# Kernel tuning notes

Measured on AMD Instinct MI355X. Metric: run time of the kernel, lower is better.

Reference implementation:

```python
import jax, jax.numpy as jnp
import numpy as np

B, N, DIM = 4, 2048, 512
HEADS, DK = 8, 64
SCALE = DK ** -0.5


def setup_inputs() -> dict:
    key = jax.random.key(0)
    k1, k2, k3, k4 = jax.random.split(key, 4)
    x = jax.random.normal(k1, (B, N, DIM), dtype=jnp.float32)
    # nn.Linear(dim, dim_key*heads, bias=False): y = x @ W.T; store W already transposed
    Wq = jax.random.normal(k2, (DIM, HEADS * DK), dtype=jnp.float32) * (DIM ** -0.5)
    Wk = jax.random.normal(k3, (DIM, HEADS * DK), dtype=jnp.float32) * (DIM ** -0.5)
    rel_content_bias = jax.random.normal(k4, (1, HEADS, 1, DK), dtype=jnp.float32)
    return {"x": x, "Wq": Wq, "Wk": Wk, "rel_content_bias": rel_content_bias}


def _split_heads(t, h):
    # [b, n, h*d] -> [b, h, n, d]
    b, n, hd = t.shape
    return t.reshape(b, n, h, hd // h).transpose(0, 2, 1, 3)


def reference(x, Wq, Wk, rel_content_bias):
    q = _split_heads(x @ Wq, HEADS) * SCALE          # [b, h, n, dk]
    k = _split_heads(x @ Wk, HEADS)                  # [b, h, n, dk]
    v = _split_heads(x, HEADS)                       # [b, h, n, dim/h]
    logits = jnp.einsum('bhid,bhjd->bhij', q + rel_content_bias, k)
    attn = jax.nn.sigmoid(logits)                    # no softmax normalization
    out = jnp.einsum('bhij,bhjd->bhid', attn, v)     # [b, h, n, dim/h]
    b, h, n, d = out.shape
    return out.transpose(0, 2, 1, 3).reshape(b, n, h * d)
```

## Files before the change

### kernel.cpp

```cpp
#include <hip/hip_runtime.h>
#include <hip/hip_bf16.h>
#include <stdint.h>

#define BB 4
#define NN 2048
#define DIMD 512
#define HH 8
#define DKK 64
#define MTOT (BB * NN)
constexpr float SCALE = 0.125f;
constexpr float L2E = 1.44269504089f;

typedef __attribute__((ext_vector_type(4))) float f32x4;
typedef __attribute__((ext_vector_type(2))) float f32x2;
typedef __attribute__((ext_vector_type(8))) short bf16x8;
typedef __attribute__((ext_vector_type(4))) _Float16 f16x4;
typedef __attribute__((ext_vector_type(8))) _Float16 f16x8;
typedef __attribute__((ext_vector_type(2))) __fp16 fp16v2;
typedef __attribute__((ext_vector_type(4))) __fp16 fp16v4;
typedef __attribute__((ext_vector_type(2))) unsigned int u32x2;

union pack8 { unsigned short s[8]; uint4 v; };
union fragu { u32x2 h[2]; bf16x8 v; };
union cat8u { f16x4 h[2]; f16x8 v; };

__device__ __forceinline__ unsigned short f2bf(float f) {
  union { float f; uint32_t u; } v; v.f = f;
  uint32_t u = v.u;
  return (unsigned short)((u + 0x7FFFu + ((u >> 16) & 1u)) >> 16);
}

__device__ __forceinline__ unsigned short f2h(float f) {
  union { _Float16 h; unsigned short u; } c; c.h = (_Float16)f;
  return c.u;
}

__device__ __forceinline__ bf16x8 ld_frag(const unsigned short* p) {
  fragu f;
  f.h[0] = *(const u32x2*)p;
  f.h[1] = *(const u32x2*)(p + 4);
  return f.v;
}
__device__ __forceinline__ void st8(unsigned short* p, uint4 v) {
  *(u32x2*)p = (u32x2){v.x, v.y};
  *(u32x2*)(p + 4) = (u32x2){v.z, v.w};
}

__device__ __forceinline__ f16x8 cat8(f16x4 a, f16x4 b) {
  cat8u u; u.h[0] = a; u.h[1] = b; return u.v;
}

__device__ __forceinline__ int kperm(int j) {
  return (j & 96) | ((j & 4) << 2) | ((j & 24) >> 1) | (j & 3);
}

__device__ __forceinline__ f16x4 sig_pack(f32x4 sv) {
  float e0 = __builtin_amdgcn_exp2f(-__builtin_fabsf(sv[0]));
  float e1 = __builtin_amdgcn_exp2f(-__builtin_fabsf(sv[1]));
  float e2 = __builtin_amdgcn_exp2f(-__builtin_fabsf(sv[2]));
  float e3 = __builtin_amdgcn_exp2f(-__builtin_fabsf(sv[3]));
  const f32x2 c3 = {-0.22184f, -0.22184f};
  const f32x2 c2 = {0.66550f, 0.66550f};
  const f32x2 c1 = {-0.94280f, -0.94280f};
  const f32x2 c0 = {0.49826f, 0.49826f};
  f32x2 eA = {e0, e1}, eB = {e2, e3};
  f32x2 pA = __builtin_elementwise_fma(
      __builtin_elementwise_fma(__builtin_elementwise_fma(c3, eA, c2), eA, c1),
      eA, c0);
  f32x2 pB = __builtin_elementwise_fma(
      __builtin_elementwise_fma(__builtin_elementwise_fma(c3, eB, c2), eB, c1),
      eB, c0);
  float r0 = __builtin_copysignf(pA.x, sv[0]);
  float r1 = __builtin_copysignf(pA.y, sv[1]);
  float r2 = __builtin_copysignf(pB.x, sv[2]);
  float r3 = __builtin_copysignf(pB.y, sv[3]);
  fp16v2 lo = __builtin_amdgcn_cvt_pkrtz(r0, r1);
  fp16v2 hi = __builtin_amdgcn_cvt_pkrtz(r2, r3);
  fp16v4 p;
  p.x = lo.x; p.y = lo.y; p.z = hi.x; p.w = hi.y;
  return __builtin_bit_cast(f16x4, p);
}

__global__ __launch_bounds__(256) void prep(const float* __restrict__ x,
                                            const float* __restrict__ wq,
                                            const float* __restrict__ wk,
                                            unsigned short* __restrict__ xtf,
                                            unsigned short* __restrict__ wtq,
                                            unsigned short* __restrict__ wtk,
                                            float* __restrict__ vsum_p) {
  const int bx = blockIdx.x, tid = threadIdx.x;
  if (bx < 256) {
    __shared__ float Pred[4][64];
    int q = bx;
    int b = q >> 6, r = q & 63;
    int dt = r >> 3, nt = r & 7;
    int dl = tid & 63, c = tid >> 6;
    int d = dt * 64 + dl;
    int n0 = nt * 256 + c * 64;
    const float* xp = x + ((size_t)b * NN + n0) * DIMD + d;
    unsigned short* dp = xtf + ((size_t)b * DIMD + d) * NN + n0;
    float s = 0.f;
#pragma unroll
    for (int g = 0; g < 8; g++) {
      pack8 pa;
#pragma unroll
      for (int k = 0; k < 8; k++) {
        float v = xp[(size_t)(g * 8 + k) * DIMD];
        s += v;
        pa.s[k] = f2h(v);
      }
      *(uint4*)(dp + g * 8) = pa.v;
    }
    Pred[c][dl] = s;
    __syncthreads();
    if (c == 0) {
      float t = Pred[0][dl] + Pred[1][dl] + Pred[2][dl] + Pred[3][dl];
      vsum_p[((size_t)b * 8 + nt) * DIMD + d] = t;
    }
  } else {
    __shared__ __align__(16) unsigned short T[64][68];
    int q = bx - 256;
    const float* w = (q >= 64) ? wk : wq;
    unsigned short* wt = (q >= 64) ? wtk : wtq;
    int r = q & 63;
    int kt = r >> 3, nt = r & 7;
    const int k0 = kt * 64, n0 = nt * 64;
#pragma unroll
    for (int rr = 0; rr < 16; rr++) {
      int idx = tid + rr * 256;
      int kl = idx >> 6, nl = idx & 63;
      T[nl][kl] = f2bf(w[(size_t)(k0 + kl) * DIMD + n0 + nl]);
    }
    __syncthreads();
#pragma unroll
    for (int rr = 0; rr < 2; rr++) {
      int idx = tid + rr * 256;
      int nl = idx >> 3, c = idx & 7;
      fragu f;
      f.h[0] = *(const u32x2*)&T[nl][c * 8];
      f.h[1] = *(const u32x2*)&T[nl][c * 8 + 4];
      uint4 v;
      v.x = f.h[0].x; v.y = f.h[0].y; v.z = f.h[1].x; v.w = f.h[1].y;
      *(uint4*)(wt + (size_t)(n0 + nl) * DIMD + k0 + c * 8) = v;
    }
  }
}

__global__ __launch_bounds__(512, 4) void qk_gemm(const float* __restrict__ x,
                                                  const unsigned short* __restrict__ wtq,
                                                  const unsigned short* __restrict__ wtk,
                                                  const float* __restrict__ bias,
                                                  unsigned short* __restrict__ qout,
                                                  unsigned short* __restrict__ kout) {
  __shared__ __align__(16) unsigned short Als[128][68];
  __shared__ __align__(16) unsigned short Bls[128][68];
  const int mb = blockIdx.x, nb = blockIdx.y;
  const bool isQ = (nb < 4);
  const unsigned short* wt = isQ ? wtq : wtk;
  unsigned short* outp = isQ ? qout : kout;
  const int n0 = (nb & 3) * 128, m0 = mb * 128;
  const int tid = threadIdx.x;
  const int wave = tid >> 6, lane = tid & 63;
  const int quad = lane >> 4, l16 = lane & 15;
  const int wm = wave >> 2, wn = wave & 3;

  f32x4 acc[4][2];
#pragma unroll
  for (int a = 0; a < 4; a++)
#pragma unroll
    for (int c = 0; c < 2; c++) acc[a][c] = (f32x4){0.f, 0.f, 0.f, 0.f};

  const int srow[2] = {tid >> 3, (tid + 512) >> 3};
  const int scol = (tid & 7) * 8;
  uint4 pa[2], pb[2];

  auto loadA = [&](int r, int k0) -> uint4 {
    const float* ap = x + (size_t)(m0 + srow[r]) * DIMD + k0 + scol;
    float4 a = *(const float4*)ap;
    float4 b = *(const float4*)(ap + 4);
    pack8 p;
    p.s[0] = f2bf(a.x); p.s[1] = f2bf(a.y); p.s[2] = f2bf(a.z); p.s[3] = f2bf(a.w);
    p.s[4] = f2bf(b.x); p.s[5] = f2bf(b.y); p.s[6] = f2bf(b.z); p.s[7] = f2bf(b.w);
    return p.v;
  };

#pragma unroll
  for (int r = 0; r < 2; r++) {
    pa[r] = loadA(r, 0);
    pb[r] = *(const uint4*)(wt + (size_t)(n0 + srow[r]) * DIMD + scol);
  }

  for (int k0 = 0; k0 < DIMD; k0 += 64) {
    __syncthreads();
#pragma unroll
    for (int r = 0; r < 2; r++) {
      st8(&Als[srow[r]][scol], pa[r]);
      st8(&Bls[srow[r]][scol], pb[r]);
    }
    __syncthreads();
    if (k0 + 64 < DIMD) {
#pragma unroll
      for (int r = 0; r < 2; r++) {
        pa[r] = loadA(r, k0 + 64);
        pb[r] = *(const uint4*)(wt + (size_t)(n0 + srow[r]) * DIMD + k0 + 64 + scol);
      }
    }
#pragma unroll
    for (int ks = 0; ks < 2; ks++) {
      bf16x8 af[4], bfr[2];
#pragma unroll
      for (int t = 0; t < 4; t++)
        af[t] = ld_frag(&Als[wm * 64 + t * 16 + l16][quad * 8 + ks * 32]);
#pragma unroll
      for (int t = 0; t < 2; t++)
        bfr[t] = ld_frag(&Bls[wn * 32 + t * 16 + l16][quad * 8 + ks * 32]);
#pragma unroll
      for (int tm = 0; tm < 4; tm++)
#pragma unroll
        for (int tn = 0; tn < 2; tn++)
          acc[tm][tn] =
              __builtin_amdgcn_mfma_f32_16x16x32_bf16(af[tm], bfr[tn], acc[tm][tn], 0, 0, 0);
    }
  }
#pragma unroll
  for (int tm = 0; tm < 4; tm++) {
#pragma unroll
    for (int tn = 0; tn < 2; tn++) {
      int gcol = n0 + wn * 32 + tn * 16 + l16;
      float bl = isQ ? bias[gcol] * L2E : 0.f;
#pragma unroll
      for (int r = 0; r < 4; r++) {
        int row = m0 + wm * 64 + tm * 16 + quad * 4 + r;
        float v = acc[tm][tn][r];
        if (isQ) v = v * (SCALE * L2E) + bl;
        outp[(size_t)row * DIMD + gcol] = f2bf(v);
      }
    }
  }
}

__global__ __launch_bounds__(512, 4) void attn(const unsigned short* __restrict__ qb,
                                               const unsigned short* __restrict__ kb,
                                               const unsigned short* __restrict__ xtf,
                                               const float* __restrict__ vsum_p,
                                               float* __restrict__ out) {
  __shared__ __align__(16) char smem[68608];
  unsigned short* Kall = (unsigned short*)smem;
  unsigned short* Vall = Kall + 2 * 128 * 68;
  float* R0 = (float*)smem;

  const int bh = blockIdx.x, it = blockIdx.y;
  const int b = bh >> 3, h = bh & 7;
  const int i0 = it * 128;
  const int tid = threadIdx.x;
  const int lane = tid & 63;
  const int grp = tid >> 8;
  const int wv = (tid >> 6) & 3;
  const int gtid = tid & 255;
  const int quad = lane >> 4, l16 = lane & 15;

  bf16x8 qf[2][2];
  int irow[2];
#pragma unroll
  for (int s_ = 0; s_ < 2; s_++) {
    irow[s_] = i0 + wv * 32 + s_ * 16 + l16;
    const unsigned short* qp = qb + ((size_t)b * NN + irow[s_]) * DIMD + h * DKK + quad * 8;
    qf[s_][0] = *(const bf16x8*)qp;
    qf[s_][1] = *(const bf16x8*)(qp + 32);
  }

  f32x4 o[2][4];
#pragma unroll
  for (int s_ = 0; s_ < 2; s_++)
#pragma unroll
    for (int td = 0; td < 4; td++) o[s_][td] = (f32x4){0.f, 0.f, 0.f, 0.f};

  const unsigned short* kbase = kb + (size_t)b * NN * DIMD + h * DKK;
  const unsigned short* vbase = xtf + ((size_t)b * DIMD + h * DKK) * NN;
  unsigned short* Kg = Kall + grp * (128 * 68);
  unsigned short* Vg = Vall + grp * (64 * 132);
  const int jbase = grp * 1024;

  const int krow = gtid >> 3, kcol = (gtid & 7) * 8;
  const int vrow = gtid >> 4, vcol = (gtid & 15) * 8;
  uint4 pk[4], pv[4];

  auto prefetch = [&](int t) {
    const int jb = jbase + t * 128;
#pragma unroll
    for (int r = 0; r < 4; r++) {
      pk[r] = *(const uint4*)(kbase + (size_t)(jb + krow + 32 * r) * DIMD + kcol);
      pv[r] = *(const uint4*)(vbase + (size_t)(vrow + 16 * r) * NN + jb + vcol);
    }
  };
  prefetch(0);

  for (int itr = 0; itr < 8; itr++) {
    __syncthreads();
#pragma unroll
    for (int r = 0; r < 4; r++) {
      st8(&Kg[kperm(krow + 32 * r) * 68 + kcol], pk[r]);
      st8(&Vg[(vrow + 16 * r) * 132 + vcol], pv[r]);
    }
    __syncthreads();
    if (itr < 7) prefetch(itr + 1);

    __builtin_amdgcn_s_setprio(1);
#pragma unroll
    for (int a = 0; a < 4; a++) {
      bf16x8 ke0 = ld_frag(&Kg[((2 * a) * 16 + l16) * 68 + quad * 8]);
      bf16x8 ke1 = ld_frag(&Kg[((2 * a) * 16 + l16) * 68 + quad * 8 + 32]);
      bf16x8 ko0 = ld_frag(&Kg[((2 * a + 1) * 16 + l16) * 68 + quad * 8]);
      bf16x8 ko1 = ld_frag(&Kg[((2 * a + 1) * 16 + l16) * 68 + quad * 8 + 32]);
      f16x8 pf[2];
#pragma unroll
      for (int s_ = 0; s_ < 2; s_++) {
        f32x4 se = (f32x4){0.f, 0.f, 0.f, 0.f};
        f32x4 so = (f32x4){0.f, 0.f, 0.f, 0.f};
        se = __builtin_amdgcn_mfma_f32_16x16x32_bf16(ke0, qf[s_][0], se, 0, 0, 0);
        se = __builtin_amdgcn_mfma_f32_16x16x32_bf16(ke1, qf[s_][1], se, 0, 0, 0);
        so = __builtin_amdgcn_mfma_f32_16x16x32_bf16(ko0, qf[s_][0], so, 0, 0, 0);
        so = __builtin_amdgcn_mfma_f32_16x16x32_bf16(ko1, qf[s_][1], so, 0, 0, 0);
        pf[s_] = cat8(sig_pack(se), sig_pack(so));
      }
#pragma unroll
      for (int td = 0; td < 4; td++) {
        f16x8 vf = __builtin_bit_cast(
            f16x8, ld_frag(&Vg[(td * 16 + l16) * 132 + a * 32 + quad * 8]));
        o[0][td] = __builtin_amdgcn_mfma_f32_16x16x32_f16(vf, pf[0], o[0][td], 0, 0, 0);
        o[1][td] = __builtin_amdgcn_mfma_f32_16x16x32_f16(vf, pf[1], o[1][td], 0, 0, 0);
      }
    }
    __builtin_amdgcn_s_setprio(0);
  }

  __syncthreads();
  if (grp == 1) {
#pragma unroll
    for (int s_ = 0; s_ < 2; s_++)
#pragma unroll
      for (int td = 0; td < 4; td++) {
        int base = (wv * 32 + s_ * 16 + l16) * 66 + td * 16 + quad * 4;
        *(f32x2*)&R0[base] = (f32x2){o[s_][td][0], o[s_][td][1]};
        *(f32x2*)&R0[base + 2] = (f32x2){o[s_][td][2], o[s_][td][3]};
      }
  }
  __syncthreads();
  if (grp == 0) {
    const float* vp = vsum_p + (size_t)b * 8 * DIMD + h * DKK;
    f32x4 vs[4];
#pragma unroll
    for (int td = 0; td < 4; td++) {
      f32x4 a = (f32x4){0.f, 0.f, 0.f, 0.f};
#pragma unroll
      for (int p = 0; p < 8; p++) {
        f32x4 t = *(const f32x4*)&vp[(size_t)p * DIMD + td * 16 + quad * 4];
        a[0] += t[0]; a[1] += t[1]; a[2] += t[2]; a[3] += t[3];
      }
      vs[td] = a;
    }
#pragma unroll
    for (int s_ = 0; s_ < 2; s_++) {
#pragma unroll
      for (int td = 0; td < 4; td++) {
        int base = (wv * 32 + s_ * 16 + l16) * 66 + td * 16 + quad * 4;
        f32x2 a = *(const f32x2*)&R0[base];
        f32x2 c = *(const f32x2*)&R0[base + 2];
        o[s_][td][0] += a.x + 0.5f * vs[td][0];
        o[s_][td][1] += a.y + 0.5f * vs[td][1];
        o[s_][td][2] += c.x + 0.5f * vs[td][2];
        o[s_][td][3] += c.y + 0.5f * vs[td][3];
        float* op = out + ((size_t)b * NN + irow[s_]) * DIMD + h * DKK + td * 16 + quad * 4;
        *(f32x4*)op = o[s_][td];
      }
    }
  }
}

extern "C" void kernel_launch(void* const* d_in, const int* in_sizes, int n_in,
                              void* d_out, int out_size, void* d_ws, size_t ws_size,
                              hipStream_t stream) {
  const float* x = (const float*)d_in[0];
  const float* Wq = (const float*)d_in[1];
  const float* Wk = (const float*)d_in[2];
  const float* bias = (const float*)d_in[3];
  float* out = (float*)d_out;

  unsigned short* ws = (unsigned short*)d_ws;
  unsigned short* xtf = ws;
  unsigned short* wtq = xtf + (size_t)MTOT * DIMD;
  unsigned short* wtk = wtq + (size_t)DIMD * DIMD;
  unsigned short* qb = wtk + (size_t)DIMD * DIMD;
  unsigned short* kb = qb + (size_t)MTOT * DIMD;
  float* vsum_p = (float*)(kb + (size_t)MTOT * DIMD);

  prep<<<dim3(384), 256, 0, stream>>>(x, Wq, Wk, xtf, wtq, wtk, vsum_p);
  qk_gemm<<<dim3(64, 8), 512, 0, stream>>>(x, wtq, wtk, bias, qb, kb);
  attn<<<dim3(32, 16), 512, 0, stream>>>(qb, kb, xtf, vsum_p, out);
}
```

Measured before the change: 154.2 us.

## Move x transpose/vsum into GEMM launch and double-buffer K fragment loads

The x transpose to fp16 and the column-sum work move out of the prep kernel into extra blocks of the qk_gemm grid, so prep only converts the weights and that work overlaps with the GEMM. In the attention inner loop, K fragments are loaded one step ahead into alternating register sets so LDS reads overlap the MFMA work. The extra grid rows share the GEMM's launch bounds and LDS allocation, which may change occupancy, and the ping-pong buffers raise register pressure.

```diff
diff --git a/kernel.cpp b/kernel.cpp
--- a/kernel.cpp
+++ b/kernel.cpp
@@ -81,85 +81,87 @@
   return __builtin_bit_cast(f16x4, p);
 }
 
-__global__ __launch_bounds__(256) void prep(const float* __restrict__ x,
-                                            const float* __restrict__ wq,
-                                            const float* __restrict__ wk,
-                                            unsigned short* __restrict__ xtf,
-                                            unsigned short* __restrict__ wtq,
-                                            unsigned short* __restrict__ wtk,
-                                            float* __restrict__ vsum_p) {
-  const int bx = blockIdx.x, tid = threadIdx.x;
-  if (bx < 256) {
-    __shared__ float Pred[4][64];
-    int q = bx;
+__global__ __launch_bounds__(256) void prep_w(const float* __restrict__ wq,
+                                              const float* __restrict__ wk,
+                                              unsigned short* __restrict__ wtq,
+                                              unsigned short* __restrict__ wtk) {
+  __shared__ __align__(16) unsigned short T[64][68];
+  const int tid = threadIdx.x;
+  int q = blockIdx.x;
+  const float* w = (q >= 64) ? wk : wq;
+  unsigned short* wt = (q >= 64) ? wtk : wtq;
+  int r = q & 63;
+  int kt = r >> 3, nt = r & 7;
+  const int k0 = kt * 64, n0 = nt * 64;
+#pragma unroll
+  for (int rr = 0; rr < 16; rr++) {
+    int idx = tid + rr * 256;
+    int kl = idx >> 6, nl = idx & 63;
+    T[nl][kl] = f2bf(w[(size_t)(k0 + kl) * DIMD + n0 + nl]);
+  }
+  __syncthreads();
+#pragma unroll
+  for (int rr = 0; rr < 2; rr++) {
+    int idx = tid + rr * 256;
+    int nl = idx >> 3, c = idx & 7;
+    fragu f;
+    f.h[0] = *(const u32x2*)&T[nl][c * 8];
+    f.h[1] = *(const u32x2*)&T[nl][c * 8 + 4];
+    uint4 v;
+    v.x = f.h[0].x; v.y = f.h[0].y; v.z = f.h[1].x; v.w = f.h[1].y;
+    *(uint4*)(wt + (size_t)(n0 + nl) * DIMD + k0 + c * 8) = v;
+  }
+}
+
+__global__ __launch_bounds__(512, 4) void qk_gemm(const float* __restrict__ x,
+                                                  const unsigned short* __restrict__ wtq,
+                                                  const unsigned short* __restrict__ wtk,
+                                                  const float* __restrict__ bias,
+                                                  unsigned short* __restrict__ qout,
+                                                  unsigned short* __restrict__ kout,
+                                                  unsigned short* __restrict__ xtf,
+                                                  float* __restrict__ vsum_p) {
+  const int mb = blockIdx.x, nb = blockIdx.y;
+  const int tid = threadIdx.x;
+
+  if (nb >= 8) {
+    __shared__ float Pred[2][4][64];
+    const int g = tid >> 8, t = tid & 255;
+    int q = (mb * 2 + (nb - 8)) * 2 + g;
     int b = q >> 6, r = q & 63;
     int dt = r >> 3, nt = r & 7;
-    int dl = tid & 63, c = tid >> 6;
+    int dl = t & 63, c = t >> 6;
     int d = dt * 64 + dl;
     int n0 = nt * 256 + c * 64;
     const float* xp = x + ((size_t)b * NN + n0) * DIMD + d;
     unsigned short* dp = xtf + ((size_t)b * DIMD + d) * NN + n0;
     float s = 0.f;
 #pragma unroll
-    for (int g = 0; g < 8; g++) {
+    for (int gg = 0; gg < 8; gg++) {
       pack8 pa;
 #pragma unroll
       for (int k = 0; k < 8; k++) {
-        float v = xp[(size_t)(g * 8 + k) * DIMD];
+        float v = xp[(size_t)(gg * 8 + k) * DIMD];
         s += v;
         pa.s[k] = f2h(v);
       }
-      *(uint4*)(dp + g * 8) = pa.v;
-    }
-    Pred[c][dl] = s;
+      *(uint4*)(dp + gg * 8) = pa.v;
+    }
+    Pred[g][c][dl] = s;
     __syncthreads();
     if (c == 0) {
-      float t = Pred[0][dl] + Pred[1][dl] + Pred[2][dl] + Pred[3][dl];
-      vsum_p[((size_t)b * 8 + nt) * DIMD + d] = t;
-    }
-  } else {
-    __shared__ __align__(16) unsigned short T[64][68];
-    int q = bx - 256;
-    const float* w = (q >= 64) ? wk : wq;
-    unsigned short* wt = (q >= 64) ? wtk : wtq;
-    int r = q & 63;
-    int kt = r >> 3, nt = r & 7;
-    const int k0 = kt * 64, n0 = nt * 64;
-#pragma unroll
-    for (int rr = 0; rr < 16; rr++) {
-      int idx = tid + rr * 256;
-      int kl = idx >> 6, nl = idx & 63;
-      T[nl][kl] = f2bf(w[(size_t)(k0 + kl) * DIMD + n0 + nl]);
-    }
-    __syncthreads();
-#pragma unroll
-    for (int rr = 0; rr < 2; rr++) {
-      int idx = tid + rr * 256;
-      int nl = idx >> 3, c = idx & 7;
-      fragu f;
-      f.h[0] = *(const u32x2*)&T[nl][c * 8];
-      f.h[1] = *(const u32x2*)&T[nl][c * 8 + 4];
-      uint4 v;
-      v.x = f.h[0].x; v.y = f.h[0].y; v.z = f.h[1].x; v.w = f.h[1].y;
-      *(uint4*)(wt + (size_t)(n0 + nl) * DIMD + k0 + c * 8) = v;
-    }
-  }
-}
-
-__global__ __launch_bounds__(512, 4) void qk_gemm(const float* __restrict__ x,
-                                                  const unsigned short* __restrict__ wtq,
-                                                  const unsigned short* __restrict__ wtk,
-                                                  const float* __restrict__ bias,
-                                                  unsigned short* __restrict__ qout,
-                                                  unsigned short* __restrict__ kout) {
+      float tt = Pred[g][0][dl] + Pred[g][1][dl] + Pred[g][2][dl] + Pred[g][3][dl];
+      vsum_p[((size_t)b * 8 + nt) * DIMD + d] = tt;
+    }
+    return;
+  }
+
   __shared__ __align__(16) unsigned short Als[128][68];
   __shared__ __align__(16) unsigned short Bls[128][68];
-  const int mb = blockIdx.x, nb = blockIdx.y;
   const bool isQ = (nb < 4);
   const unsigned short* wt = isQ ? wtq : wtk;
   unsigned short* outp = isQ ? qout : kout;
   const int n0 = (nb & 3) * 128, m0 = mb * 128;
-  const int tid = threadIdx.x;
   const int wave = tid >> 6, lane = tid & 63;
   const int quad = lane >> 4, l16 = lane & 15;
   const int wm = wave >> 2, wn = wave & 3;
@@ -295,6 +297,33 @@
   };
   prefetch(0);
 
+  auto loadK = [&](int a, bf16x8* kf) {
+    kf[0] = ld_frag(&Kg[((2 * a) * 16 + l16) * 68 + quad * 8]);
+    kf[1] = ld_frag(&Kg[((2 * a) * 16 + l16) * 68 + quad * 8 + 32]);
+    kf[2] = ld_frag(&Kg[((2 * a + 1) * 16 + l16) * 68 + quad * 8]);
+    kf[3] = ld_frag(&Kg[((2 * a + 1) * 16 + l16) * 68 + quad * 8 + 32]);
+  };
+  auto computeA = [&](int a, const bf16x8* kf) {
+    f16x8 pf[2];
+#pragma unroll
+    for (int s_ = 0; s_ < 2; s_++) {
+      f32x4 se = (f32x4){0.f, 0.f, 0.f, 0.f};
+      f32x4 so = (f32x4){0.f, 0.f, 0.f, 0.f};
+      se = __builtin_amdgcn_mfma_f32_16x16x32_bf16(kf[0], qf[s_][0], se, 0, 0, 0);
+      se = __builtin_amdgcn_mfma_f32_16x16x32_bf16(kf[1], qf[s_][1], se, 0, 0, 0);
+      so = __builtin_amdgcn_mfma_f32_16x16x32_bf16(kf[2], qf[s_][0], so, 0, 0, 0);
+      so = __builtin_amdgcn_mfma_f32_16x16x32_bf16(kf[3], qf[s_][1], so, 0, 0, 0);
+      pf[s_] = cat8(sig_pack(se), sig_pack(so));
+    }
+#pragma unroll
+    for (int td = 0; td < 4; td++) {
+      f16x8 vf = __builtin_bit_cast(
+          f16x8, ld_frag(&Vg[(td * 16 + l16) * 132 + a * 32 + quad * 8]));
+      o[0][td] = __builtin_amdgcn_mfma_f32_16x16x32_f16(vf, pf[0], o[0][td], 0, 0, 0);
+      o[1][td] = __builtin_amdgcn_mfma_f32_16x16x32_f16(vf, pf[1], o[1][td], 0, 0, 0);
+    }
+  };
+
   for (int itr = 0; itr < 8; itr++) {
     __syncthreads();
 #pragma unroll
@@ -306,31 +335,15 @@
     if (itr < 7) prefetch(itr + 1);
 
     __builtin_amdgcn_s_setprio(1);
-#pragma unroll
-    for (int a = 0; a < 4; a++) {
-      bf16x8 ke0 = ld_frag(&Kg[((2 * a) * 16 + l16) * 68 + quad * 8]);
-      bf16x8 ke1 = ld_frag(&Kg[((2 * a) * 16 + l16) * 68 + quad * 8 + 32]);
-      bf16x8 ko0 = ld_frag(&Kg[((2 * a + 1) * 16 + l16) * 68 + quad * 8]);
-      bf16x8 ko1 = ld_frag(&Kg[((2 * a + 1) * 16 + l16) * 68 + quad * 8 + 32]);
-      f16x8 pf[2];
-#pragma unroll
-      for (int s_ = 0; s_ < 2; s_++) {
-        f32x4 se = (f32x4){0.f, 0.f, 0.f, 0.f};
-        f32x4 so = (f32x4){0.f, 0.f, 0.f, 0.f};
-        se = __builtin_amdgcn_mfma_f32_16x16x32_bf16(ke0, qf[s_][0], se, 0, 0, 0);
-        se = __builtin_amdgcn_mfma_f32_16x16x32_bf16(ke1, qf[s_][1], se, 0, 0, 0);
-        so = __builtin_amdgcn_mfma_f32_16x16x32_bf16(ko0, qf[s_][0], so, 0, 0, 0);
-        so = __builtin_amdgcn_mfma_f32_16x16x32_bf16(ko1, qf[s_][1], so, 0, 0, 0);
-        pf[s_] = cat8(sig_pack(se), sig_pack(so));
-      }
-#pragma unroll
-      for (int td = 0; td < 4; td++) {
-        f16x8 vf = __builtin_bit_cast(
-            f16x8, ld_frag(&Vg[(td * 16 + l16) * 132 + a * 32 + quad * 8]));
-        o[0][td] = __builtin_amdgcn_mfma_f32_16x16x32_f16(vf, pf[0], o[0][td], 0, 0, 0);
-        o[1][td] = __builtin_amdgcn_mfma_f32_16x16x32_f16(vf, pf[1], o[1][td], 0, 0, 0);
-      }
-    }
+    bf16x8 kfA[4], kfB[4];
+    loadK(0, kfA);
+    loadK(1, kfB);
+    computeA(0, kfA);
+    loadK(2, kfA);
+    computeA(1, kfB);
+    loadK(3, kfB);
+    computeA(2, kfA);
+    computeA(3, kfB);
     __builtin_amdgcn_s_setprio(0);
   }
 
@@ -394,7 +407,7 @@
   unsigned short* kb = qb + (size_t)MTOT * DIMD;
   float* vsum_p = (float*)(kb + (size_t)MTOT * DIMD);
 
-  prep<<<dim3(384), 256, 0, stream>>>(x, Wq, Wk, xtf, wtq, wtk, vsum_p);
-  qk_gemm<<<dim3(64, 8), 512, 0, stream>>>(x, wtq, wtk, bias, qb, kb);
+  prep_w<<<dim3(128), 256, 0, stream>>>(Wq, Wk, wtq, wtk);
+  qk_gemm<<<dim3(64, 10), 512, 0, stream>>>(x, wtq, wtk, bias, qb, kb, xtf, vsum_p);
   attn<<<dim3(32, 16), 512, 0, stream>>>(qb, kb, xtf, vsum_p, out);
 }
```

After: 160.2 us. 3.9% more time.
